# Kernel tuning notes

Hardware: AMD Instinct MI355X
Metric: run time of the kernel (lower is better)

The kernel has to match this reference:

```python
import jax, jax.numpy as jnp
import numpy as np

N = 100000       # num nodes
E = 1600000      # num edges
IN_DIM = 256
OUT_DIM = 64
RANK = 3         # hard-coded LoRA rank in the module


def setup_inputs() -> dict:
    key = jax.random.key(0)
    k1, k2, k3, k4 = jax.random.split(key, 4)
    x = jax.random.normal(k1, (N, IN_DIM), dtype=jnp.float32)
    edge_index = jax.random.randint(k2, (2, E), 0, N, dtype=jnp.int64)
    # Learned params. Original init is B=0 / A~N(0,0.01) / bias=0; use random
    # nonzero values so the reference exercises the full datapath.
    W_B = jax.random.normal(k3, (RANK, IN_DIM), dtype=jnp.float32) * 0.05   # Linear(in_dim, r).weight
    W_A = jax.random.normal(k4, (OUT_DIM, RANK), dtype=jnp.float32) * 0.01  # Linear(r, out_dim).weight
    bias = jnp.zeros((OUT_DIM,), dtype=jnp.float32)
    return {"x": x, "edge_index": edge_index, "W_B": W_B, "W_A": W_A, "bias": bias}


def _propagate2(h, edge_index):
    # PyG add_remaining_self_loops == drop existing self loops, then add a
    # self loop for every node. Implemented with static shapes via masking.
    row, col = edge_index[0], edge_index[1]
    mask = row != col                                    # [E] non-self-loop edges
    deg = jax.ops.segment_sum(mask.astype(h.dtype), col, num_segments=N) + 1.0  # +1 self loop
    dinv = deg ** -0.5                                   # deg >= 1, safe
    w = jnp.where(mask, dinv[row] * dinv[col], 0.0)      # [E]
    out = jax.ops.segment_sum(w[:, None] * h[row], col, num_segments=N)  # gather-scale-scatter
    out = out + (dinv * dinv)[:, None] * h               # self-loop contribution
    return out


def reference(x, edge_index, W_B, W_A, bias):
    h = (x @ W_B.T) @ W_A.T            # LoRA: [N, r] -> [N, out_dim]
    return _propagate2(h, edge_index) + bias
```

## Files before the change

kernel.cpp:

```cpp
#include <hip/hip_runtime.h>
#include <hip/hip_bf16.h>


#define RANK 3
#define IN_DIM 256
#define OUT_DIM 64

#define NB    256
#define BS    392
#define CAP2  8192
#define CHUNK 4096

__global__ void k1_zproj_bin(const float* __restrict__ x,
                             const float* __restrict__ WB,
                             float4* __restrict__ z4, int N,
                             const int* __restrict__ idx, int E, int nsample,
                             unsigned* __restrict__ recs, int* __restrict__ gcur,
                             int nbin) {
    __shared__ int s_hist[NB];
    __shared__ int s_lbase[NB];
    __shared__ int s_base[NB];
    __shared__ int s_rank[NB];
    __shared__ int s_wsum[4];
    __shared__ int s_nz;
    __shared__ unsigned s_buf[CHUNK];

    if ((int)blockIdx.x < nbin) {
        if (threadIdx.x == 0) s_nz = 0;
        { int t = threadIdx.x; s_hist[t] = 0; s_rank[t] = 0; }
        __syncthreads();
        int nz = 0;
        for (int i = threadIdx.x; i < nsample; i += 256) nz |= idx[2 * i + 1];
        if (nz) s_nz = 1;
        __syncthreads();
        const int stride = (s_nz == 0) ? 2 : 1;
        const int* rowp = idx;
        const int* colp = idx + (size_t)E * stride;
        const int e0 = blockIdx.x * CHUNK;

        int er[16], ec[16];
        #pragma unroll
        for (int k = 0; k < 16; ++k) {
            int e = e0 + k * 256 + (int)threadIdx.x;
            er[k] = 0; ec[k] = 0;
            if (e < E) {
                if (stride == 2) {
                    er[k] = reinterpret_cast<const int2*>(rowp)[e].x;
                    ec[k] = reinterpret_cast<const int2*>(colp)[e].x;
                } else {
                    er[k] = rowp[e];
                    ec[k] = colp[e];
                }
            }
        }
        #pragma unroll
        for (int k = 0; k < 16; ++k)
            if (er[k] != ec[k]) atomicAdd(&s_hist[ec[k] / BS], 1);
        __syncthreads();

        {
            int t = threadIdx.x;
            int v = s_hist[t];
            int incl = v;
            #pragma unroll
            for (int d = 1; d < 64; d <<= 1) {
                int o = __shfl_up(incl, d);
                if ((t & 63) >= d) incl += o;
            }
            if ((t & 63) == 63) s_wsum[t >> 6] = incl;
            __syncthreads();
            int woff = 0;
            #pragma unroll
            for (int w = 0; w < 4; ++w) if (w < (t >> 6)) woff += s_wsum[w];
            s_lbase[t] = woff + incl - v;
            s_base[t]  = v ? atomicAdd(&gcur[t], v) : 0;
        }
        __syncthreads();

        #pragma unroll
        for (int k = 0; k < 16; ++k) {
            if (er[k] != ec[k]) {
                int b = ec[k] / BS;
                int pos = s_lbase[b] + atomicAdd(&s_rank[b], 1);
                s_buf[pos] = ((unsigned)er[k] << 9) | (unsigned)(ec[k] - b * BS);
            }
        }
        __syncthreads();

        int total = s_lbase[NB - 1] + s_hist[NB - 1];
        for (int i = threadIdx.x; i < total; i += 256) {
            int lo = 0, hi = NB - 1;
            #pragma unroll
            for (int s = 0; s < 8; ++s) {
                int mid = (lo + hi + 1) >> 1;
                if (s_lbase[mid] <= i) lo = mid; else hi = mid - 1;
            }
            int rel = s_base[lo] + (i - s_lbase[lo]);
            if (rel < CAP2)
                recs[(size_t)lo * CAP2 + rel] = s_buf[i];
        }
        return;
    }

    int gtid = (blockIdx.x - nbin) * blockDim.x + threadIdx.x;
    int node = gtid >> 4;
    int l = threadIdx.x & 15;
    if (node >= N) return;

    const float4* xr = reinterpret_cast<const float4*>(x + (size_t)node * IN_DIM);
    const float4* wb0 = reinterpret_cast<const float4*>(WB);
    const float4* wb1 = reinterpret_cast<const float4*>(WB + IN_DIM);
    const float4* wb2 = reinterpret_cast<const float4*>(WB + 2 * IN_DIM);

    float p0 = 0.f, p1 = 0.f, p2 = 0.f;
    #pragma unroll
    for (int j = 0; j < 4; ++j) {
        int c = j * 16 + l;
        float4 xv = xr[c];
        float4 w0 = wb0[c];
        float4 w1 = wb1[c];
        float4 w2 = wb2[c];
        p0 += xv.x * w0.x + xv.y * w0.y + xv.z * w0.z + xv.w * w0.w;
        p1 += xv.x * w1.x + xv.y * w1.y + xv.z * w1.z + xv.w * w1.w;
        p2 += xv.x * w2.x + xv.y * w2.y + xv.z * w2.z + xv.w * w2.w;
    }
    #pragma unroll
    for (int m = 8; m > 0; m >>= 1) {
        p0 += __shfl_xor(p0, m);
        p1 += __shfl_xor(p1, m);
        p2 += __shfl_xor(p2, m);
    }
    if (l == 0) z4[node] = make_float4(p0, p1, p2, 0.0f);
}

__global__ void __launch_bounds__(512) k2_zw(
        const unsigned* __restrict__ recs, const int* __restrict__ gcur,
        const float4* __restrict__ z4, float4* __restrict__ zw, int N) {
    __shared__ int s_deg[BS];
    int b = blockIdx.x;
    for (int j = threadIdx.x; j < BS; j += 512) s_deg[j] = 0;
    __syncthreads();
    int cnt = gcur[b]; if (cnt > CAP2) cnt = CAP2;
    const unsigned* rb = recs + (size_t)b * CAP2;
    for (int i = threadIdx.x; i < cnt; i += 512)
        atomicAdd(&s_deg[rb[i] & 511u], 1);
    __syncthreads();
    for (int j = threadIdx.x; j < BS; j += 512) {
        int n = b * BS + j;
        if (n >= N) break;
        float di = rsqrtf((float)s_deg[j] + 1.0f);
        float4 zn = z4[n];
        zw[n] = make_float4(di * zn.x, di * zn.y, di * zn.z, di);
    }
}

__global__ void __launch_bounds__(1024) k3_aggout(
        const unsigned* __restrict__ recs, const int* __restrict__ gcur,
        const float4* __restrict__ zw,
        const float* __restrict__ WA,
        const float* __restrict__ bias,
        float* __restrict__ out, int N) {
    __shared__ float s_agg[BS * 3];
    __shared__ float s_wa0[64], s_wa1[64], s_wa2[64], s_bb[64];
    int b = blockIdx.x;

    for (int j = threadIdx.x; j < BS * 3; j += 1024) s_agg[j] = 0.0f;
    if (threadIdx.x < 64) {
        int j = threadIdx.x;
        s_wa0[j] = WA[j * 3 + 0];
        s_wa1[j] = WA[j * 3 + 1];
        s_wa2[j] = WA[j * 3 + 2];
        s_bb[j]  = bias[j];
    }
    __syncthreads();

    int cnt = gcur[b]; if (cnt > CAP2) cnt = CAP2;
    const unsigned* rb = recs + (size_t)b * CAP2;
    for (int i = threadIdx.x; i < cnt; i += 1024) {
        unsigned rc = rb[i];
        int cl = (int)(rc & 511u);
        float4 zr = zw[rc >> 9];
        atomicAdd(&s_agg[cl * 3 + 0], zr.x);
        atomicAdd(&s_agg[cl * 3 + 1], zr.y);
        atomicAdd(&s_agg[cl * 3 + 2], zr.z);
    }
    __syncthreads();

    if (threadIdx.x < BS) {
        int n = b * BS + (int)threadIdx.x;
        if (n < N) {
            float4 zn = zw[n];
            float di = zn.w;
            s_agg[threadIdx.x * 3 + 0] = di * (s_agg[threadIdx.x * 3 + 0] + zn.x);
            s_agg[threadIdx.x * 3 + 1] = di * (s_agg[threadIdx.x * 3 + 1] + zn.y);
            s_agg[threadIdx.x * 3 + 2] = di * (s_agg[threadIdx.x * 3 + 2] + zn.z);
        }
    }
    __syncthreads();

    for (int i = threadIdx.x; i < BS * 16; i += 1024) {
        int nl = i >> 4, j4 = (i & 15) << 2;
        int n = b * BS + nl;
        if (n >= N) continue;
        float a0 = s_agg[nl * 3 + 0], a1 = s_agg[nl * 3 + 1], a2 = s_agg[nl * 3 + 2];
        float4 o;
        o.x = a0 * s_wa0[j4+0] + a1 * s_wa1[j4+0] + a2 * s_wa2[j4+0] + s_bb[j4+0];
        o.y = a0 * s_wa0[j4+1] + a1 * s_wa1[j4+1] + a2 * s_wa2[j4+1] + s_bb[j4+1];
        o.z = a0 * s_wa0[j4+2] + a1 * s_wa1[j4+2] + a2 * s_wa2[j4+2] + s_bb[j4+2];
        o.w = a0 * s_wa0[j4+3] + a1 * s_wa1[j4+3] + a2 * s_wa2[j4+3] + s_bb[j4+3];
        *reinterpret_cast<float4*>(out + (size_t)n * OUT_DIM + j4) = o;
    }
}

__global__ void detect_kernel(const int* __restrict__ idx, int nsample, int* flag) {
    __shared__ int s_nz;
    if (threadIdx.x == 0) s_nz = 0;
    __syncthreads();
    int nz = 0;
    for (int i = threadIdx.x; i < nsample; i += blockDim.x) nz |= idx[2 * i + 1];
    if (nz) s_nz = 1;
    __syncthreads();
    if (threadIdx.x == 0) *flag = (s_nz == 0) ? 1 : 0;
}
__global__ void deg_kernel(const int* __restrict__ idx, int E,
                           const int* __restrict__ flag, float* __restrict__ deg) {
    int stride = (*flag) ? 2 : 1;
    const int* rowp = idx;
    const int* colp = idx + (size_t)E * stride;
    int step = gridDim.x * blockDim.x;
    for (int e = blockIdx.x * blockDim.x + threadIdx.x; e < E; e += step) {
        int r = rowp[(size_t)e * stride];
        int c = colp[(size_t)e * stride];
        if (r != c) atomicAdd(&deg[c], 1.0f);
    }
}
__global__ void dinv_self_kernel(const float4* __restrict__ z4, const float* __restrict__ deg,
                                 float* __restrict__ dinv, float* __restrict__ agg, int N) {
    int n = blockIdx.x * blockDim.x + threadIdx.x;
    if (n >= N) return;
    float d = deg[n] + 1.0f;
    float di = rsqrtf(d);
    dinv[n] = di;
    float w = 1.0f / d;
    float4 zn = z4[n];
    agg[(size_t)n * 3 + 0] = w * zn.x;
    agg[(size_t)n * 3 + 1] = w * zn.y;
    agg[(size_t)n * 3 + 2] = w * zn.z;
}
__global__ void scatter_kernel(const int* __restrict__ idx, int E,
                               const int* __restrict__ flag,
                               const float4* __restrict__ z4,
                               const float* __restrict__ dinv,
                               float* __restrict__ agg) {
    int stride = (*flag) ? 2 : 1;
    const int* rowp = idx;
    const int* colp = idx + (size_t)E * stride;
    int step = gridDim.x * blockDim.x;
    for (int e = blockIdx.x * blockDim.x + threadIdx.x; e < E; e += step) {
        int r = rowp[(size_t)e * stride];
        int c = colp[(size_t)e * stride];
        if (r != c) {
            float w = dinv[r] * dinv[c];
            float4 zr = z4[r];
            atomicAdd(&agg[(size_t)c * 3 + 0], w * zr.x);
            atomicAdd(&agg[(size_t)c * 3 + 1], w * zr.y);
            atomicAdd(&agg[(size_t)c * 3 + 2], w * zr.z);
        }
    }
}
__global__ void out_kernel(const float* __restrict__ agg,
                           const float* __restrict__ WA,
                           const float* __restrict__ bias,
                           float* __restrict__ out, int N) {
    int t = blockIdx.x * blockDim.x + threadIdx.x;
    int n = t >> 6;
    int j = t & 63;
    if (n >= N) return;
    float a0 = agg[(size_t)n * 3 + 0];
    float a1 = agg[(size_t)n * 3 + 1];
    float a2 = agg[(size_t)n * 3 + 2];
    out[(size_t)n * OUT_DIM + j] =
        a0 * WA[j * 3 + 0] + a1 * WA[j * 3 + 1] + a2 * WA[j * 3 + 2] + bias[j];
}

extern "C" void kernel_launch(void* const* d_in, const int* in_sizes, int n_in,
                              void* d_out, int out_size, void* d_ws, size_t ws_size,
                              hipStream_t stream) {
    const float* x    = (const float*)d_in[0];
    const int*   idx  = (const int*)d_in[1];
    const float* WB   = (const float*)d_in[2];
    const float* WA   = (const float*)d_in[3];
    const float* bias = (const float*)d_in[4];
    float* out = (float*)d_out;

    const int N = in_sizes[0] / IN_DIM;
    const int E = in_sizes[1] / 2;

    auto align256 = [](size_t o) { return (o + 255) & ~(size_t)255; };
    char* ws = (char*)d_ws;
    size_t off = 0;
    int*    flag = (int*)(ws + off);    off = align256(off + sizeof(int));
    int*    gcur = (int*)(ws + off);    off = align256(off + NB * sizeof(int));
    float4* z4   = (float4*)(ws + off); off = align256(off + (size_t)N * sizeof(float4));
    float4* zw   = (float4*)(ws + off); off = align256(off + (size_t)N * sizeof(float4));
    float*  dinv = (float*)(ws + off);  off = align256(off + (size_t)N * sizeof(float));
    unsigned* recs = (unsigned*)(ws + off); off = align256(off + (size_t)NB * CAP2 * sizeof(unsigned));
    float* degF = (float*)zw;
    float* aggF = (float*)recs;

    const bool fast = (N <= NB * BS) && (N < (1 << 23)) && (ws_size >= off);

    int nsample = E < 1024 ? E : 1024;

    if (fast) {
        hipMemsetAsync(gcur, 0, NB * sizeof(int), stream);
        int nbin = (E + CHUNK - 1) / CHUNK;
        int nzp  = (N + 15) / 16;
        k1_zproj_bin<<<nbin + nzp, 256, 0, stream>>>(x, WB, z4, N, idx, E, nsample,
                                                     recs, gcur, nbin);
        k2_zw<<<NB, 512, 0, stream>>>(recs, gcur, z4, zw, N);
        k3_aggout<<<NB, 1024, 0, stream>>>(recs, gcur, zw, WA, bias, out, N);
    } else {
        detect_kernel<<<1, 256, 0, stream>>>(idx, nsample, flag);
        k1_zproj_bin<<<(N + 15) / 16, 256, 0, stream>>>(x, WB, z4, N, idx, E, nsample,
                                                        (unsigned*)aggF, gcur, 0);
        hipMemsetAsync(degF, 0, (size_t)N * sizeof(float), stream);
        deg_kernel<<<2048, 256, 0, stream>>>(idx, E, flag, degF);
        dinv_self_kernel<<<(N + 255) / 256, 256, 0, stream>>>(z4, degF, dinv, aggF, N);
        scatter_kernel<<<2048, 256, 0, stream>>>(idx, E, flag, z4, dinv, aggF);
        long long total = (long long)N * OUT_DIM;
        out_kernel<<<(int)((total + 255) / 256), 256, 0, stream>>>(aggF, WA, bias, out, N);
    }
}
```

Before: 71.80 us.

## Replace global atomic bin cursors with per-chunk histogram tables and segmented reads

The binning kernel no longer reserves space in global per-bin buckets with atomics. Each chunk now writes its locally sorted records contiguously, plus a per-chunk histogram and local offsets. The consumer kernels prefix-sum those per-chunk counts for their bin and locate each record by binary search. This removes the memset, the global atomics and the CAP2 overflow truncation, at the cost of a scan preamble and a per-element binary search in k2 and k3.

```diff
diff --git a/kernel.cpp b/kernel.cpp
--- a/kernel.cpp
+++ b/kernel.cpp
@@ -8,24 +8,26 @@
 
 #define NB    256
 #define BS    392
-#define CAP2  8192
 #define CHUNK 4096
+#define NQMAX 512
 
 __global__ void k1_zproj_bin(const float* __restrict__ x,
                              const float* __restrict__ WB,
                              float4* __restrict__ z4, int N,
                              const int* __restrict__ idx, int E, int nsample,
-                             unsigned* __restrict__ recs, int* __restrict__ gcur,
+                             unsigned* __restrict__ recs,
+                             int* __restrict__ hist_t,
+                             int* __restrict__ lbase_t,
                              int nbin) {
     __shared__ int s_hist[NB];
     __shared__ int s_lbase[NB];
-    __shared__ int s_base[NB];
     __shared__ int s_rank[NB];
     __shared__ int s_wsum[4];
     __shared__ int s_nz;
     __shared__ unsigned s_buf[CHUNK];
 
-    if ((int)blockIdx.x < nbin) {
+    const int q = blockIdx.x;
+    if (q < nbin) {
         if (threadIdx.x == 0) s_nz = 0;
         { int t = threadIdx.x; s_hist[t] = 0; s_rank[t] = 0; }
         __syncthreads();
@@ -36,7 +38,7 @@
         const int stride = (s_nz == 0) ? 2 : 1;
         const int* rowp = idx;
         const int* colp = idx + (size_t)E * stride;
-        const int e0 = blockIdx.x * CHUNK;
+        const int e0 = q * CHUNK;
 
         int er[16], ec[16];
         #pragma unroll
@@ -73,7 +75,8 @@
             #pragma unroll
             for (int w = 0; w < 4; ++w) if (w < (t >> 6)) woff += s_wsum[w];
             s_lbase[t] = woff + incl - v;
-            s_base[t]  = v ? atomicAdd(&gcur[t], v) : 0;
+            hist_t[(size_t)q * NB + t]  = v;
+            lbase_t[(size_t)q * NB + t] = woff + incl - v;
         }
         __syncthreads();
 
@@ -88,21 +91,13 @@
         __syncthreads();
 
         int total = s_lbase[NB - 1] + s_hist[NB - 1];
-        for (int i = threadIdx.x; i < total; i += 256) {
-            int lo = 0, hi = NB - 1;
-            #pragma unroll
-            for (int s = 0; s < 8; ++s) {
-                int mid = (lo + hi + 1) >> 1;
-                if (s_lbase[mid] <= i) lo = mid; else hi = mid - 1;
-            }
-            int rel = s_base[lo] + (i - s_lbase[lo]);
-            if (rel < CAP2)
-                recs[(size_t)lo * CAP2 + rel] = s_buf[i];
-        }
+        unsigned* dst = recs + (size_t)q * CHUNK;
+        for (int i = threadIdx.x; i < total; i += 256)
+            dst[i] = s_buf[i];
         return;
     }
 
-    int gtid = (blockIdx.x - nbin) * blockDim.x + threadIdx.x;
+    int gtid = (q - nbin) * blockDim.x + threadIdx.x;
     int node = gtid >> 4;
     int l = threadIdx.x & 15;
     if (node >= N) return;
@@ -133,17 +128,67 @@
     if (l == 0) z4[node] = make_float4(p0, p1, p2, 0.0f);
 }
 
+__device__ __forceinline__ int seg_preamble(const int* __restrict__ hist_t,
+                                            const int* __restrict__ lbase_t,
+                                            int b, int nbin,
+                                            int* sP, int* sBase, int* s_total) {
+    if (threadIdx.x < 64) {
+        int l = threadIdx.x;
+        int h[NQMAX / 64];
+        int s = 0;
+        #pragma unroll
+        for (int k = 0; k < NQMAX / 64; ++k) {
+            int q = l * (NQMAX / 64) + k;
+            int v = (q < nbin) ? hist_t[(size_t)q * NB + b] : 0;
+            if (q < nbin) sBase[q] = lbase_t[(size_t)q * NB + b];
+            h[k] = s;
+            s += v;
+        }
+        int incl = s;
+        #pragma unroll
+        for (int d = 1; d < 64; d <<= 1) {
+            int o = __shfl_up(incl, d);
+            if (l >= d) incl += o;
+        }
+        int excl = incl - s;
+        #pragma unroll
+        for (int k = 0; k < NQMAX / 64; ++k) {
+            int q = l * (NQMAX / 64) + k;
+            if (q < NQMAX) sP[q] = excl + h[k];
+        }
+        if (l == 63) *s_total = incl;
+    }
+    __syncthreads();
+    return *s_total;
+}
+
+__device__ __forceinline__ int seg_find(const int* sP, int nbin, int j) {
+    int lo = 0, hi = nbin - 1;
+    while (lo < hi) {
+        int mid = (lo + hi + 1) >> 1;
+        if (sP[mid] <= j) lo = mid; else hi = mid - 1;
+    }
+    return lo;
+}
+
 __global__ void __launch_bounds__(512) k2_zw(
-        const unsigned* __restrict__ recs, const int* __restrict__ gcur,
-        const float4* __restrict__ z4, float4* __restrict__ zw, int N) {
+        const unsigned* __restrict__ recs,
+        const int* __restrict__ hist_t, const int* __restrict__ lbase_t,
+        const float4* __restrict__ z4, float4* __restrict__ zw,
+        int N, int nbin) {
+    __shared__ int sP[NQMAX];
+    __shared__ int sBase[NQMAX];
     __shared__ int s_deg[BS];
+    __shared__ int s_total;
     int b = blockIdx.x;
     for (int j = threadIdx.x; j < BS; j += 512) s_deg[j] = 0;
-    __syncthreads();
-    int cnt = gcur[b]; if (cnt > CAP2) cnt = CAP2;
-    const unsigned* rb = recs + (size_t)b * CAP2;
-    for (int i = threadIdx.x; i < cnt; i += 512)
-        atomicAdd(&s_deg[rb[i] & 511u], 1);
+    int total = seg_preamble(hist_t, lbase_t, b, nbin, sP, sBase, &s_total);
+
+    for (int j = threadIdx.x; j < total; j += 512) {
+        int q = seg_find(sP, nbin, j);
+        unsigned rc = recs[(size_t)q * CHUNK + sBase[q] + (j - sP[q])];
+        atomicAdd(&s_deg[rc & 511u], 1);
+    }
     __syncthreads();
     for (int j = threadIdx.x; j < BS; j += 512) {
         int n = b * BS + j;
@@ -155,29 +200,32 @@
 }
 
 __global__ void __launch_bounds__(1024) k3_aggout(
-        const unsigned* __restrict__ recs, const int* __restrict__ gcur,
+        const unsigned* __restrict__ recs,
+        const int* __restrict__ hist_t, const int* __restrict__ lbase_t,
         const float4* __restrict__ zw,
         const float* __restrict__ WA,
         const float* __restrict__ bias,
-        float* __restrict__ out, int N) {
+        float* __restrict__ out, int N, int nbin) {
+    __shared__ int sP[NQMAX];
+    __shared__ int sBase[NQMAX];
     __shared__ float s_agg[BS * 3];
     __shared__ float s_wa0[64], s_wa1[64], s_wa2[64], s_bb[64];
+    __shared__ int s_total;
     int b = blockIdx.x;
 
     for (int j = threadIdx.x; j < BS * 3; j += 1024) s_agg[j] = 0.0f;
-    if (threadIdx.x < 64) {
-        int j = threadIdx.x;
+    if (threadIdx.x >= 1024 - 64) {
+        int j = threadIdx.x - (1024 - 64);
         s_wa0[j] = WA[j * 3 + 0];
         s_wa1[j] = WA[j * 3 + 1];
         s_wa2[j] = WA[j * 3 + 2];
         s_bb[j]  = bias[j];
     }
-    __syncthreads();
-
-    int cnt = gcur[b]; if (cnt > CAP2) cnt = CAP2;
-    const unsigned* rb = recs + (size_t)b * CAP2;
-    for (int i = threadIdx.x; i < cnt; i += 1024) {
-        unsigned rc = rb[i];
+    int total = seg_preamble(hist_t, lbase_t, b, nbin, sP, sBase, &s_total);
+
+    for (int j = threadIdx.x; j < total; j += 1024) {
+        int q = seg_find(sP, nbin, j);
+        unsigned rc = recs[(size_t)q * CHUNK + sBase[q] + (j - sP[q])];
         int cl = (int)(rc & 511u);
         float4 zr = zw[rc >> 9];
         atomicAdd(&s_agg[cl * 3 + 0], zr.x);
@@ -299,31 +347,34 @@
     auto align256 = [](size_t o) { return (o + 255) & ~(size_t)255; };
     char* ws = (char*)d_ws;
     size_t off = 0;
-    int*    flag = (int*)(ws + off);    off = align256(off + sizeof(int));
-    int*    gcur = (int*)(ws + off);    off = align256(off + NB * sizeof(int));
-    float4* z4   = (float4*)(ws + off); off = align256(off + (size_t)N * sizeof(float4));
-    float4* zw   = (float4*)(ws + off); off = align256(off + (size_t)N * sizeof(float4));
-    float*  dinv = (float*)(ws + off);  off = align256(off + (size_t)N * sizeof(float));
-    unsigned* recs = (unsigned*)(ws + off); off = align256(off + (size_t)NB * CAP2 * sizeof(unsigned));
+    int*    flag   = (int*)(ws + off);    off = align256(off + sizeof(int));
+    float4* z4     = (float4*)(ws + off); off = align256(off + (size_t)N * sizeof(float4));
+    float4* zw     = (float4*)(ws + off); off = align256(off + (size_t)N * sizeof(float4));
+    float*  dinv   = (float*)(ws + off);  off = align256(off + (size_t)N * sizeof(float));
+    int*    hist_t = (int*)(ws + off);    off = align256(off + (size_t)NQMAX * NB * sizeof(int));
+    int*    lbase_t= (int*)(ws + off);    off = align256(off + (size_t)NQMAX * NB * sizeof(int));
+    unsigned* recs = (unsigned*)(ws + off); off = align256(off + (size_t)NQMAX * CHUNK * sizeof(unsigned));
     float* degF = (float*)zw;
     float* aggF = (float*)recs;
 
-    const bool fast = (N <= NB * BS) && (N < (1 << 23)) && (ws_size >= off);
+    int nbin = (E + CHUNK - 1) / CHUNK;
+    const bool fast = (N <= NB * BS) && (N < (1 << 23)) && (nbin <= NQMAX)
+                      && (ws_size >= off);
 
     int nsample = E < 1024 ? E : 1024;
 
     if (fast) {
-        hipMemsetAsync(gcur, 0, NB * sizeof(int), stream);
-        int nbin = (E + CHUNK - 1) / CHUNK;
-        int nzp  = (N + 15) / 16;
+        int nzp = (N + 15) / 16;
         k1_zproj_bin<<<nbin + nzp, 256, 0, stream>>>(x, WB, z4, N, idx, E, nsample,
-                                                     recs, gcur, nbin);
-        k2_zw<<<NB, 512, 0, stream>>>(recs, gcur, z4, zw, N);
-        k3_aggout<<<NB, 1024, 0, stream>>>(recs, gcur, zw, WA, bias, out, N);
+                                                     recs, hist_t, lbase_t, nbin);
+        k2_zw<<<NB, 512, 0, stream>>>(recs, hist_t, lbase_t, z4, zw, N, nbin);
+        k3_aggout<<<NB, 1024, 0, stream>>>(recs, hist_t, lbase_t, zw, WA, bias,
+                                           out, N, nbin);
     } else {
         detect_kernel<<<1, 256, 0, stream>>>(idx, nsample, flag);
         k1_zproj_bin<<<(N + 15) / 16, 256, 0, stream>>>(x, WB, z4, N, idx, E, nsample,
-                                                        (unsigned*)aggF, gcur, 0);
+                                                        (unsigned*)aggF, hist_t,
+                                                        lbase_t, 0);
         hipMemsetAsync(degF, 0, (size_t)N * sizeof(float), stream);
         deg_kernel<<<2048, 256, 0, stream>>>(idx, E, flag, degF);
         dinv_self_kernel<<<(N + 255) / 256, 256, 0, stream>>>(z4, degF, dinv, aggF, N);
```

After: 81.43 us. +13.4%, slower.
